# Optimization experiments

Measured on AMD Instinct MI355X. Metric: run time of the kernel, lower is better.

Reference implementation:

```python
import jax, jax.numpy as jnp
import numpy as np

MODEL_DIM = 1024
NUM_HEADS = 16
HEAD_DIM = MODEL_DIM // NUM_HEADS
WINDOW = 4


def local_mask(seq_len):
    i = jnp.arange(seq_len)
    return jnp.abs(i[:, None] - i[None, :]) <= WINDOW  # [S,S] bool


def setup_inputs() -> dict:
    key = jax.random.key(0)
    ks = jax.random.split(key, 9)
    d = MODEL_DIM
    s = 0.02
    return {
        "x": jax.random.normal(ks[0], (4, 2048, d), dtype=jnp.float32),
        "Wq": jax.random.normal(ks[1], (d, d), dtype=jnp.float32) * s,
        "bq": jnp.zeros((d,), dtype=jnp.float32),
        "Wk": jax.random.normal(ks[2], (d, d), dtype=jnp.float32) * s,
        "bk": jnp.zeros((d,), dtype=jnp.float32),
        "Wv": jax.random.normal(ks[3], (d, d), dtype=jnp.float32) * s,
        "bv": jnp.zeros((d,), dtype=jnp.float32),
        "Wo": jax.random.normal(ks[4], (d, d), dtype=jnp.float32) * s,
        "bo": jnp.zeros((d,), dtype=jnp.float32),
    }


def reference(x, Wq, bq, Wk, bk, Wv, bv, Wo, bo):
    B, S, D = x.shape
    H, Hd = NUM_HEADS, HEAD_DIM
    # linear projections (torch Linear: x @ W.T + b; here W stored pre-transposed)
    q = (x @ Wq + bq).reshape(B, S, H, Hd).transpose(0, 2, 1, 3)  # [B,H,S,Hd]
    k = (x @ Wk + bk).reshape(B, S, H, Hd).transpose(0, 2, 1, 3)
    v = (x @ Wv + bv).reshape(B, S, H, Hd).transpose(0, 2, 1, 3)
    scores = jnp.einsum("bhqd,bhkd->bhqk", q, k) / jnp.sqrt(jnp.float32(Hd))
    mask = local_mask(S)[None, None]  # [1,1,S,S]
    scores = jnp.where(mask, scores, -jnp.inf)
    weights = jax.nn.softmax(scores, axis=-1)  # [B,H,S,S]
    out = jnp.einsum("bhqk,bhkd->bhqd", weights, v)
    out = out.transpose(0, 2, 1, 3).reshape(B, S, D)
    out = out @ Wo + bo
    return (out, weights)
```

## Files before the change

kernel.cpp:

```cpp
#include <hip/hip_runtime.h>


typedef __attribute__((ext_vector_type(8))) short short8;
typedef __attribute__((ext_vector_type(4))) float f32x4;

#define B_    4
#define S_    2048
#define D_    1024
#define H_    16
#define HD_   64
#define WIN_  4
#define NROW  (B_ * S_)
#define OUT0_ELEMS  ((size_t)B_ * S_ * D_)

__device__ __forceinline__ unsigned short f2bf(float f) {
  unsigned int u = __float_as_uint(f);
  u += 0x7fffu + ((u >> 16) & 1u);
  return (unsigned short)(u >> 16);
}
__device__ __forceinline__ float bf2f(unsigned short u) {
  return __uint_as_float(((unsigned int)u) << 16);
}

__global__ __launch_bounds__(256) void xconv_k(const float* __restrict__ x,
                                               unsigned short* __restrict__ o) {
  int i = blockIdx.x * 256 + threadIdx.x;
  float4 f = reinterpret_cast<const float4*>(x)[i];
  ushort4 u;
  u.x = f2bf(f.x); u.y = f2bf(f.y); u.z = f2bf(f.z); u.w = f2bf(f.w);
  reinterpret_cast<ushort4*>(o)[i] = u;
}

__global__ __launch_bounds__(256) void wconv_k(const float* __restrict__ W0,
                                               const float* __restrict__ W1,
                                               const float* __restrict__ W2,
                                               const float* __restrict__ W3,
                                               unsigned short* __restrict__ out) {
  __shared__ float t[32][33];
  const float* Ws[4] = {W0, W1, W2, W3};
  const float* W = Ws[blockIdx.z];
  unsigned short* o = out + (size_t)blockIdx.z * D_ * D_;
  int tx = threadIdx.x;
  int ty = threadIdx.y;
  int n0 = blockIdx.x * 32, k0 = blockIdx.y * 32;
#pragma unroll
  for (int i = 0; i < 4; ++i)
    t[ty + 8 * i][tx] = W[(size_t)(k0 + ty + 8 * i) * D_ + (n0 + tx)];
  __syncthreads();
#pragma unroll
  for (int i = 0; i < 4; ++i)
    o[(size_t)(n0 + ty + 8 * i) * D_ + (k0 + tx)] = f2bf(t[tx][ty + 8 * i]);
}

#define GLD16(g, l)                                                            \
  __builtin_amdgcn_global_load_lds(                                            \
      (const __attribute__((address_space(1))) unsigned int*)(g),              \
      (__attribute__((address_space(3))) unsigned int*)(l), 16, 0, 0)

__global__ __launch_bounds__(256) void gemm_qkv_k(
    const unsigned short* __restrict__ A, const unsigned short* __restrict__ Wt,
    const float* __restrict__ bq, const float* __restrict__ bk,
    const float* __restrict__ bv, unsigned short* __restrict__ Qb,
    unsigned short* __restrict__ Kb, unsigned short* __restrict__ Vb) {
  __shared__ unsigned short As[128 * 32];
  __shared__ unsigned short Bs[128 * 32];
  const int g = blockIdx.x;
  const int o = g & 7, gg = g >> 3;
  const int row0 = (o * 8 + (gg & 7)) * 128;
  const int col0 = (gg >> 3) * 128;

  const int tid = threadIdx.x;
  const int lane = tid & 63;
  const int wid = tid >> 6;
  const int wm = wid >> 1, wn = wid & 1;

  f32x4 acc[4][4] = {};
  const int frow = lane & 15;
  const int koff = (lane >> 4) << 3;

  for (int kt = 0; kt < 32; ++kt) {
#pragma unroll
    for (int i = 0; i < 2; ++i) {
      int c = tid + (i << 8);
      int r = c >> 2;
      int kk = (c & 3) << 3;
      GLD16(A + (size_t)(row0 + r) * D_ + (kt << 5) + kk, (char*)As + c * 16);
      GLD16(Wt + (size_t)(col0 + r) * D_ + (kt << 5) + kk, (char*)Bs + c * 16);
    }
    __syncthreads();
    short8 af[4], bfr[4];
#pragma unroll
    for (int mi = 0; mi < 4; ++mi)
      af[mi] = *reinterpret_cast<const short8*>(
          &As[(wm * 64 + mi * 16 + frow) * 32 + koff]);
#pragma unroll
    for (int ni = 0; ni < 4; ++ni)
      bfr[ni] = *reinterpret_cast<const short8*>(
          &Bs[(wn * 64 + ni * 16 + frow) * 32 + koff]);
#pragma unroll
    for (int mi = 0; mi < 4; ++mi)
#pragma unroll
      for (int ni = 0; ni < 4; ++ni)
        acc[mi][ni] = __builtin_amdgcn_mfma_f32_16x16x32_bf16(
            af[mi], bfr[ni], acc[mi][ni], 0, 0, 0);
    __syncthreads();
  }

#pragma unroll
  for (int mi = 0; mi < 4; ++mi) {
#pragma unroll
    for (int ni = 0; ni < 4; ++ni) {
#pragma unroll
      for (int r = 0; r < 4; ++r) {
        int gr = row0 + wm * 64 + mi * 16 + ((lane >> 4) << 2) + r;
        int gc = col0 + wn * 64 + ni * 16 + (lane & 15);
        int z = gc >> 10;
        int ci = gc & 1023;
        float bias = (z == 0) ? bq[ci] : (z == 1) ? bk[ci] : bv[ci];
        unsigned short* outp = (z == 0) ? Qb : (z == 1) ? Kb : Vb;
        int bb = gr >> 11, s = gr & (S_ - 1);
        int h = ci >> 6, hd = ci & 63;
        outp[(((size_t)(bb * H_ + h) * S_ + s) << 6) + hd] =
            f2bf(acc[mi][ni][r] + bias);
      }
    }
  }
}

__global__ __launch_bounds__(256) void gemm_out_k(
    const unsigned short* __restrict__ A, const unsigned short* __restrict__ Bt,
    const float* __restrict__ bias, float* __restrict__ o_) {
  __shared__ unsigned short As[128 * 32];
  __shared__ unsigned short Bs[128 * 32];
  const int g = blockIdx.x;
  const int o = g & 7, gg = g >> 3;
  const int row0 = (o * 8 + (gg & 7)) * 128;
  const int col0 = (gg >> 3) * 128;

  const int tid = threadIdx.x;
  const int lane = tid & 63;
  const int wid = tid >> 6;
  const int wm = wid >> 1, wn = wid & 1;

  f32x4 acc[4][4] = {};
  const int frow = lane & 15;
  const int koff = (lane >> 4) << 3;

  for (int kt = 0; kt < 32; ++kt) {
#pragma unroll
    for (int i = 0; i < 2; ++i) {
      int c = tid + (i << 8);
      int r = c >> 2;
      int kk = (c & 3) << 3;
      GLD16(A + (size_t)(row0 + r) * D_ + (kt << 5) + kk, (char*)As + c * 16);
      GLD16(Bt + (size_t)(col0 + r) * D_ + (kt << 5) + kk, (char*)Bs + c * 16);
    }
    __syncthreads();
    short8 af[4], bfr[4];
#pragma unroll
    for (int mi = 0; mi < 4; ++mi)
      af[mi] = *reinterpret_cast<const short8*>(
          &As[(wm * 64 + mi * 16 + frow) * 32 + koff]);
#pragma unroll
    for (int ni = 0; ni < 4; ++ni)
      bfr[ni] = *reinterpret_cast<const short8*>(
          &Bs[(wn * 64 + ni * 16 + frow) * 32 + koff]);
#pragma unroll
    for (int mi = 0; mi < 4; ++mi)
#pragma unroll
      for (int ni = 0; ni < 4; ++ni)
        acc[mi][ni] = __builtin_amdgcn_mfma_f32_16x16x32_bf16(
            af[mi], bfr[ni], acc[mi][ni], 0, 0, 0);
    __syncthreads();
  }

#pragma unroll
  for (int mi = 0; mi < 4; ++mi) {
#pragma unroll
    for (int ni = 0; ni < 4; ++ni) {
#pragma unroll
      for (int r = 0; r < 4; ++r) {
        int gr = row0 + wm * 64 + mi * 16 + ((lane >> 4) << 2) + r;
        int gc = col0 + wn * 64 + ni * 16 + (lane & 15);
        o_[(size_t)gr * D_ + gc] = acc[mi][ni][r] + bias[gc];
      }
    }
  }
}

__global__ __launch_bounds__(256) void attn_k(const unsigned short* __restrict__ Q,
                                              const unsigned short* __restrict__ K,
                                              const unsigned short* __restrict__ V,
                                              float* __restrict__ wout,
                                              unsigned short* __restrict__ attn) {
  int lane = threadIdx.x & 63;
  int wid = threadIdx.x >> 6;
  int row = blockIdx.x * 4 + wid;
  int s = row & (S_ - 1);
  int bh = row >> 11;
  int b = bh >> 4, h = bh & 15;
  float qd = bf2f(Q[(size_t)row * HD_ + lane]);
  const unsigned short* Kb = K + (size_t)bh * S_ * HD_;
  const unsigned short* Vb = V + (size_t)bh * S_ * HD_;

  float sc[9];
#pragma unroll
  for (int j = 0; j < 9; ++j) {
    int ks = s - WIN_ + j;
    bool ok = (ks >= 0) && (ks < S_);
    float v = ok ? qd * bf2f(Kb[(size_t)ks * HD_ + lane]) : 0.f;
#pragma unroll
    for (int off = 32; off > 0; off >>= 1) v += __shfl_xor(v, off, 64);
    sc[j] = ok ? v * 0.125f : -INFINITY;
  }
  float m = sc[0];
#pragma unroll
  for (int j = 1; j < 9; ++j) m = fmaxf(m, sc[j]);
  float w[9];
  float sum = 0.f;
#pragma unroll
  for (int j = 0; j < 9; ++j) { w[j] = __expf(sc[j] - m); sum += w[j]; }
  float inv = 1.f / sum;
#pragma unroll
  for (int j = 0; j < 9; ++j) w[j] *= inv;

  float o = 0.f;
#pragma unroll
  for (int j = 0; j < 9; ++j) {
    int ks = s - WIN_ + j;
    if (ks >= 0 && ks < S_) o += w[j] * bf2f(Vb[(size_t)ks * HD_ + lane]);
  }
  attn[((size_t)(b * S_ + s)) * D_ + h * HD_ + lane] = f2bf(o);

  f32x4* rowp = reinterpret_cast<f32x4*>(wout + (size_t)row * S_);
  const int lo = s - WIN_;
  const int hi = s + WIN_;
#pragma unroll
  for (int i = 0; i < 8; ++i) {
    int f = lane + (i << 6);
    int c0 = f << 2;
    f32x4 v4 = {0.f, 0.f, 0.f, 0.f};
    if (c0 + 3 >= lo && c0 <= hi) {
#pragma unroll
      for (int e = 0; e < 4; ++e) {
        int d = c0 + e - lo;
        float val = 0.f;
#pragma unroll
        for (int j = 0; j < 9; ++j)
          if (d == j) val = w[j];
        v4[e] = val;
      }
    }
    __builtin_nontemporal_store(v4, rowp + f);
  }
}

extern "C" void kernel_launch(void* const* d_in, const int* in_sizes, int n_in,
                              void* d_out, int out_size, void* d_ws,
                              size_t ws_size, hipStream_t stream) {
  const float* x = (const float*)d_in[0];
  const float* Wq = (const float*)d_in[1];
  const float* bq = (const float*)d_in[2];
  const float* Wk = (const float*)d_in[3];
  const float* bk = (const float*)d_in[4];
  const float* Wv = (const float*)d_in[5];
  const float* bv = (const float*)d_in[6];
  const float* Wo = (const float*)d_in[7];
  const float* bo = (const float*)d_in[8];
  float* out = (float*)d_out;
  float* wout = out + OUT0_ELEMS;

  char* ws = (char*)d_ws;
  unsigned short* x_bf = (unsigned short*)(ws);
  unsigned short* Wt = (unsigned short*)(ws + (16ull << 20));
  unsigned short* Qb = (unsigned short*)(ws + (24ull << 20));
  unsigned short* Kb = (unsigned short*)(ws + (40ull << 20));
  unsigned short* Vb = (unsigned short*)(ws + (56ull << 20));
  unsigned short* attn = (unsigned short*)(ws + (72ull << 20));

  xconv_k<<<NROW * D_ / 1024, 256, 0, stream>>>(x, x_bf);
  wconv_k<<<dim3(32, 32, 4), dim3(32, 8), 0, stream>>>(Wq, Wk, Wv, Wo, Wt);
  gemm_qkv_k<<<1536, 256, 0, stream>>>(x_bf, Wt, bq, bk, bv, Qb, Kb, Vb);
  attn_k<<<(B_ * H_ * S_) / 4, 256, 0, stream>>>(Qb, Kb, Vb, wout, attn);
  gemm_out_k<<<512, 256, 0, stream>>>(attn, Wt + (size_t)3 * D_ * D_, bo, out);
}
```

Measured before the change: 282.6 us.

## Overlap weight-matrix zero fill with QKV GEMM and widen GEMM K-tile with LDS swizzle

Moves most of the zero stores for the dense attention-weights output out of the attention kernel and into the QKV GEMM main loop, so those memory-bound writes can overlap MFMA work. The attention kernel now writes only the window chunks plus the remaining zero chunks. Both GEMMs switch to a 64-wide K tile with an XOR-swizzled LDS layout, halving the number of barrier iterations and reducing bank conflicts. The trade-off is more LDS per block, and the GEMM now shares memory bandwidth with the large store stream.

```diff
diff --git a/kernel.cpp b/kernel.cpp
--- a/kernel.cpp
+++ b/kernel.cpp
@@ -12,6 +12,8 @@
 #define WIN_  4
 #define NROW  (B_ * S_)
 #define OUT0_ELEMS  ((size_t)B_ * S_ * D_)
+#define TOTAL_CH  67108864ull
+#define ZQKV_CH   18874368ull
 
 __device__ __forceinline__ unsigned short f2bf(float f) {
   unsigned int u = __float_as_uint(f);
@@ -20,6 +22,19 @@
 }
 __device__ __forceinline__ float bf2f(unsigned short u) {
   return __uint_as_float(((unsigned int)u) << 16);
+}
+
+__device__ __forceinline__ void zstore(f32x4* __restrict__ woutv, size_t g) {
+  int row = (int)(g >> 9);
+  int f = (int)(g & 511);
+  int s = row & (S_ - 1);
+  int f0 = (s > WIN_) ? ((s - WIN_) >> 2) : 0;
+  int hi = (s + WIN_ < S_ - 1) ? (s + WIN_) : (S_ - 1);
+  int f1 = hi >> 2;
+  if (f < f0 || f > f1) {
+    f32x4 z = {0.f, 0.f, 0.f, 0.f};
+    __builtin_nontemporal_store(z, woutv + g);
+  }
 }
 
 __global__ __launch_bounds__(256) void xconv_k(const float* __restrict__ x,
@@ -61,9 +76,10 @@
     const unsigned short* __restrict__ A, const unsigned short* __restrict__ Wt,
     const float* __restrict__ bq, const float* __restrict__ bk,
     const float* __restrict__ bv, unsigned short* __restrict__ Qb,
-    unsigned short* __restrict__ Kb, unsigned short* __restrict__ Vb) {
-  __shared__ unsigned short As[128 * 32];
-  __shared__ unsigned short Bs[128 * 32];
+    unsigned short* __restrict__ Kb, unsigned short* __restrict__ Vb,
+    float* __restrict__ wout) {
+  __shared__ unsigned short As[128 * 64];
+  __shared__ unsigned short Bs[128 * 64];
   const int g = blockIdx.x;
   const int o = g & 7, gg = g >> 3;
   const int row0 = (o * 8 + (gg & 7)) * 128;
@@ -73,36 +89,49 @@
   const int lane = tid & 63;
   const int wid = tid >> 6;
   const int wm = wid >> 1, wn = wid & 1;
+  f32x4* woutv = (f32x4*)wout;
 
   f32x4 acc[4][4] = {};
   const int frow = lane & 15;
-  const int koff = (lane >> 4) << 3;
-
-  for (int kt = 0; kt < 32; ++kt) {
-#pragma unroll
-    for (int i = 0; i < 2; ++i) {
+  const int cpb = lane >> 4;
+
+  for (int kt = 0; kt < 16; ++kt) {
+#pragma unroll
+    for (int j = 0; j < 3; ++j)
+      zstore(woutv, (size_t)(kt * 3 + j) * 393216u + (unsigned)g * 256u + tid);
+#pragma unroll
+    for (int i = 0; i < 4; ++i) {
       int c = tid + (i << 8);
-      int r = c >> 2;
-      int kk = (c & 3) << 3;
-      GLD16(A + (size_t)(row0 + r) * D_ + (kt << 5) + kk, (char*)As + c * 16);
-      GLD16(Wt + (size_t)(col0 + r) * D_ + (kt << 5) + kk, (char*)Bs + c * 16);
+      int r = c >> 3;
+      int jj = (c & 7) ^ (r & 7);
+      GLD16(A + (size_t)(row0 + r) * D_ + (kt << 6) + (jj << 3),
+            (char*)As + c * 16);
+      GLD16(Wt + (size_t)(col0 + r) * D_ + (kt << 6) + (jj << 3),
+            (char*)Bs + c * 16);
     }
     __syncthreads();
-    short8 af[4], bfr[4];
-#pragma unroll
-    for (int mi = 0; mi < 4; ++mi)
-      af[mi] = *reinterpret_cast<const short8*>(
-          &As[(wm * 64 + mi * 16 + frow) * 32 + koff]);
-#pragma unroll
-    for (int ni = 0; ni < 4; ++ni)
-      bfr[ni] = *reinterpret_cast<const short8*>(
-          &Bs[(wn * 64 + ni * 16 + frow) * 32 + koff]);
-#pragma unroll
-    for (int mi = 0; mi < 4; ++mi)
-#pragma unroll
-      for (int ni = 0; ni < 4; ++ni)
-        acc[mi][ni] = __builtin_amdgcn_mfma_f32_16x16x32_bf16(
-            af[mi], bfr[ni], acc[mi][ni], 0, 0, 0);
+#pragma unroll
+    for (int ks = 0; ks < 2; ++ks) {
+      short8 af[4], bfr[4];
+#pragma unroll
+      for (int mi = 0; mi < 4; ++mi) {
+        int row = wm * 64 + mi * 16 + frow;
+        int swz = (ks * 4 + cpb) ^ (row & 7);
+        af[mi] = *reinterpret_cast<const short8*>((char*)As + row * 128 + swz * 16);
+      }
+#pragma unroll
+      for (int ni = 0; ni < 4; ++ni) {
+        int row = wn * 64 + ni * 16 + frow;
+        int swz = (ks * 4 + cpb) ^ (row & 7);
+        bfr[ni] = *reinterpret_cast<const short8*>((char*)Bs + row * 128 + swz * 16);
+      }
+#pragma unroll
+      for (int mi = 0; mi < 4; ++mi)
+#pragma unroll
+        for (int ni = 0; ni < 4; ++ni)
+          acc[mi][ni] = __builtin_amdgcn_mfma_f32_16x16x32_bf16(
+              af[mi], bfr[ni], acc[mi][ni], 0, 0, 0);
+    }
     __syncthreads();
   }
 
@@ -130,8 +159,8 @@
 __global__ __launch_bounds__(256) void gemm_out_k(
     const unsigned short* __restrict__ A, const unsigned short* __restrict__ Bt,
     const float* __restrict__ bias, float* __restrict__ o_) {
-  __shared__ unsigned short As[128 * 32];
-  __shared__ unsigned short Bs[128 * 32];
+  __shared__ unsigned short As[128 * 64];
+  __shared__ unsigned short Bs[128 * 64];
   const int g = blockIdx.x;
   const int o = g & 7, gg = g >> 3;
   const int row0 = (o * 8 + (gg & 7)) * 128;
@@ -144,33 +173,42 @@
 
   f32x4 acc[4][4] = {};
   const int frow = lane & 15;
-  const int koff = (lane >> 4) << 3;
-
-  for (int kt = 0; kt < 32; ++kt) {
-#pragma unroll
-    for (int i = 0; i < 2; ++i) {
+  const int cpb = lane >> 4;
+
+  for (int kt = 0; kt < 16; ++kt) {
+#pragma unroll
+    for (int i = 0; i < 4; ++i) {
       int c = tid + (i << 8);
-      int r = c >> 2;
-      int kk = (c & 3) << 3;
-      GLD16(A + (size_t)(row0 + r) * D_ + (kt << 5) + kk, (char*)As + c * 16);
-      GLD16(Bt + (size_t)(col0 + r) * D_ + (kt << 5) + kk, (char*)Bs + c * 16);
+      int r = c >> 3;
+      int jj = (c & 7) ^ (r & 7);
+      GLD16(A + (size_t)(row0 + r) * D_ + (kt << 6) + (jj << 3),
+            (char*)As + c * 16);
+      GLD16(Bt + (size_t)(col0 + r) * D_ + (kt << 6) + (jj << 3),
+            (char*)Bs + c * 16);
     }
     __syncthreads();
-    short8 af[4], bfr[4];
-#pragma unroll
-    for (int mi = 0; mi < 4; ++mi)
-      af[mi] = *reinterpret_cast<const short8*>(
-          &As[(wm * 64 + mi * 16 + frow) * 32 + koff]);
-#pragma unroll
-    for (int ni = 0; ni < 4; ++ni)
-      bfr[ni] = *reinterpret_cast<const short8*>(
-          &Bs[(wn * 64 + ni * 16 + frow) * 32 + koff]);
-#pragma unroll
-    for (int mi = 0; mi < 4; ++mi)
-#pragma unroll
-      for (int ni = 0; ni < 4; ++ni)
-        acc[mi][ni] = __builtin_amdgcn_mfma_f32_16x16x32_bf16(
-            af[mi], bfr[ni], acc[mi][ni], 0, 0, 0);
+#pragma unroll
+    for (int ks = 0; ks < 2; ++ks) {
+      short8 af[4], bfr[4];
+#pragma unroll
+      for (int mi = 0; mi < 4; ++mi) {
+        int row = wm * 64 + mi * 16 + frow;
+        int swz = (ks * 4 + cpb) ^ (row & 7);
+        af[mi] = *reinterpret_cast<const short8*>((char*)As + row * 128 + swz * 16);
+      }
+#pragma unroll
+      for (int ni = 0; ni < 4; ++ni) {
+        int row = wn * 64 + ni * 16 + frow;
+        int swz = (ks * 4 + cpb) ^ (row & 7);
+        bfr[ni] = *reinterpret_cast<const short8*>((char*)Bs + row * 128 + swz * 16);
+      }
+#pragma unroll
+      for (int mi = 0; mi < 4; ++mi)
+#pragma unroll
+        for (int ni = 0; ni < 4; ++ni)
+          acc[mi][ni] = __builtin_amdgcn_mfma_f32_16x16x32_bf16(
+              af[mi], bfr[ni], acc[mi][ni], 0, 0, 0);
+    }
     __syncthreads();
   }
 
@@ -232,26 +270,30 @@
   }
   attn[((size_t)(b * S_ + s)) * D_ + h * HD_ + lane] = f2bf(o);
 
+  const int lo = s - WIN_;
+  const int hiq = (s + WIN_ < S_ - 1) ? (s + WIN_) : (S_ - 1);
+  const int f0 = (s > WIN_) ? ((s - WIN_) >> 2) : 0;
+  const int f1 = hiq >> 2;
   f32x4* rowp = reinterpret_cast<f32x4*>(wout + (size_t)row * S_);
-  const int lo = s - WIN_;
-  const int hi = s + WIN_;
-#pragma unroll
-  for (int i = 0; i < 8; ++i) {
-    int f = lane + (i << 6);
-    int c0 = f << 2;
-    f32x4 v4 = {0.f, 0.f, 0.f, 0.f};
-    if (c0 + 3 >= lo && c0 <= hi) {
-#pragma unroll
-      for (int e = 0; e < 4; ++e) {
-        int d = c0 + e - lo;
-        float val = 0.f;
-#pragma unroll
-        for (int j = 0; j < 9; ++j)
-          if (d == j) val = w[j];
-        v4[e] = val;
-      }
-    }
-    __builtin_nontemporal_store(v4, rowp + f);
+  if (lane <= f1 - f0) {
+    f32x4 v4;
+#pragma unroll
+    for (int e = 0; e < 4; ++e) {
+      int d = ((f0 + lane) << 2) + e - lo;
+      float val = 0.f;
+#pragma unroll
+      for (int j = 0; j < 9; ++j)
+        if (d == j) val = w[j];
+      v4[e] = val;
+    }
+    __builtin_nontemporal_store(v4, rowp + f0 + lane);
+  }
+
+  unsigned int gtid = blockIdx.x * 256u + threadIdx.x;
+#pragma unroll
+  for (int k2 = 0; k2 < 6; ++k2) {
+    size_t g = ZQKV_CH + (size_t)k2 * 8388608u + gtid;
+    if (g < TOTAL_CH) zstore((f32x4*)wout, g);
   }
 }
 
@@ -280,7 +322,7 @@
 
   xconv_k<<<NROW * D_ / 1024, 256, 0, stream>>>(x, x_bf);
   wconv_k<<<dim3(32, 32, 4), dim3(32, 8), 0, stream>>>(Wq, Wk, Wv, Wo, Wt);
-  gemm_qkv_k<<<1536, 256, 0, stream>>>(x_bf, Wt, bq, bk, bv, Qb, Kb, Vb);
+  gemm_qkv_k<<<1536, 256, 0, stream>>>(x_bf, Wt, bq, bk, bv, Qb, Kb, Vb, wout);
   attn_k<<<(B_ * H_ * S_) / 4, 256, 0, stream>>>(Qb, Kb, Vb, wout, attn);
   gemm_out_k<<<512, 256, 0, stream>>>(attn, Wt + (size_t)3 * D_ * D_, bo, out);
 }
```

New measurement: 285.6 us. Within noise of the previous version (+1.1%).

## Store Q/K/V in row-major [B,S,D] layout and add nontemporal output stores

Applied to the files above, without the earlier changes.

The QKV projection epilogue now writes Q, K and V row-major as [B*S, D] instead of the head-transposed [B,H,S,Hd] layout. It also selects the bias and output pointer once per block rather than per element. The attention kernel indexes Q/K/V with a stride of D to match. The output GEMM uses nontemporal stores for the large fp32 result. The aim is contiguous epilogue writes and cheaper index math, at the cost of strided per-row reads in attention, and the nontemporal hint may or may not help.

```diff
diff --git a/kernel.cpp b/kernel.cpp
--- a/kernel.cpp
+++ b/kernel.cpp
@@ -57,6 +57,8 @@
       (const __attribute__((address_space(1))) unsigned int*)(g),              \
       (__attribute__((address_space(3))) unsigned int*)(l), 16, 0, 0)
 
+#define MFMA16(a, b, c) __builtin_amdgcn_mfma_f32_16x16x32_bf16(a, b, c, 0, 0, 0)
+
 __global__ __launch_bounds__(256) void gemm_qkv_k(
     const unsigned short* __restrict__ A, const unsigned short* __restrict__ Wt,
     const float* __restrict__ bq, const float* __restrict__ bk,
@@ -101,11 +103,14 @@
     for (int mi = 0; mi < 4; ++mi)
 #pragma unroll
       for (int ni = 0; ni < 4; ++ni)
-        acc[mi][ni] = __builtin_amdgcn_mfma_f32_16x16x32_bf16(
-            af[mi], bfr[ni], acc[mi][ni], 0, 0, 0);
-    __syncthreads();
-  }
-
+        acc[mi][ni] = MFMA16(af[mi], bfr[ni], acc[mi][ni]);
+    __syncthreads();
+  }
+
+  const int z = col0 >> 10;
+  const float* bias = (z == 0) ? bq : (z == 1) ? bk : bv;
+  unsigned short* outp = (z == 0) ? Qb : (z == 1) ? Kb : Vb;
+  const int cb = col0 & 1023;
 #pragma unroll
   for (int mi = 0; mi < 4; ++mi) {
 #pragma unroll
@@ -113,15 +118,8 @@
 #pragma unroll
       for (int r = 0; r < 4; ++r) {
         int gr = row0 + wm * 64 + mi * 16 + ((lane >> 4) << 2) + r;
-        int gc = col0 + wn * 64 + ni * 16 + (lane & 15);
-        int z = gc >> 10;
-        int ci = gc & 1023;
-        float bias = (z == 0) ? bq[ci] : (z == 1) ? bk[ci] : bv[ci];
-        unsigned short* outp = (z == 0) ? Qb : (z == 1) ? Kb : Vb;
-        int bb = gr >> 11, s = gr & (S_ - 1);
-        int h = ci >> 6, hd = ci & 63;
-        outp[(((size_t)(bb * H_ + h) * S_ + s) << 6) + hd] =
-            f2bf(acc[mi][ni][r] + bias);
+        int ci = cb + wn * 64 + ni * 16 + (lane & 15);
+        outp[(size_t)gr * D_ + ci] = f2bf(acc[mi][ni][r] + bias[ci]);
       }
     }
   }
@@ -169,8 +167,7 @@
     for (int mi = 0; mi < 4; ++mi)
 #pragma unroll
       for (int ni = 0; ni < 4; ++ni)
-        acc[mi][ni] = __builtin_amdgcn_mfma_f32_16x16x32_bf16(
-            af[mi], bfr[ni], acc[mi][ni], 0, 0, 0);
+        acc[mi][ni] = MFMA16(af[mi], bfr[ni], acc[mi][ni]);
     __syncthreads();
   }
 
@@ -182,7 +179,8 @@
       for (int r = 0; r < 4; ++r) {
         int gr = row0 + wm * 64 + mi * 16 + ((lane >> 4) << 2) + r;
         int gc = col0 + wn * 64 + ni * 16 + (lane & 15);
-        o_[(size_t)gr * D_ + gc] = acc[mi][ni][r] + bias[gc];
+        __builtin_nontemporal_store(acc[mi][ni][r] + bias[gc],
+                                    &o_[(size_t)gr * D_ + gc]);
       }
     }
   }
@@ -199,16 +197,15 @@
   int s = row & (S_ - 1);
   int bh = row >> 11;
   int b = bh >> 4, h = bh & 15;
-  float qd = bf2f(Q[(size_t)row * HD_ + lane]);
-  const unsigned short* Kb = K + (size_t)bh * S_ * HD_;
-  const unsigned short* Vb = V + (size_t)bh * S_ * HD_;
+  const size_t rbase = (size_t)(b * S_) * D_ + h * HD_ + lane;
+  float qd = bf2f(Q[rbase + (size_t)s * D_]);
 
   float sc[9];
 #pragma unroll
   for (int j = 0; j < 9; ++j) {
     int ks = s - WIN_ + j;
     bool ok = (ks >= 0) && (ks < S_);
-    float v = ok ? qd * bf2f(Kb[(size_t)ks * HD_ + lane]) : 0.f;
+    float v = ok ? qd * bf2f(K[rbase + (size_t)ks * D_]) : 0.f;
 #pragma unroll
     for (int off = 32; off > 0; off >>= 1) v += __shfl_xor(v, off, 64);
     sc[j] = ok ? v * 0.125f : -INFINITY;
@@ -228,9 +225,9 @@
 #pragma unroll
   for (int j = 0; j < 9; ++j) {
     int ks = s - WIN_ + j;
-    if (ks >= 0 && ks < S_) o += w[j] * bf2f(Vb[(size_t)ks * HD_ + lane]);
-  }
-  attn[((size_t)(b * S_ + s)) * D_ + h * HD_ + lane] = f2bf(o);
+    if (ks >= 0 && ks < S_) o += w[j] * bf2f(V[rbase + (size_t)ks * D_]);
+  }
+  attn[(size_t)(b * S_ + s) * D_ + h * HD_ + lane] = f2bf(o);
 
   f32x4* rowp = reinterpret_cast<f32x4*>(wout + (size_t)row * S_);
   const int lo = s - WIN_;
```

New measurement: 296.2 us. 4.8% more time.
